# Optimization experiments

Measured on AMD Instinct MI355X. Metric: run time of the kernel, lower is better.

The kernel has to match this reference:

```python
import jax, jax.numpy as jnp
import numpy as np

D_MODEL = 2048
D_STATE = 16
EXPAND = 2
D_INNER = D_MODEL * EXPAND
BATCH = 2048
LN_EPS = 1e-5


def setup_inputs() -> dict:
    key = jax.random.key(0)
    ks = jax.random.split(key, 8)
    x = jax.random.normal(ks[0], (BATCH, D_MODEL), dtype=jnp.float32)
    h = jax.random.normal(ks[1], (BATCH, D_INNER, D_STATE), dtype=jnp.float32)
    # Learned parameters (Linear weights stored as (out, in), torch convention)
    W_in = jax.random.normal(ks[2], (2 * D_INNER, D_MODEL), dtype=jnp.float32) / np.sqrt(D_MODEL)
    W_xp = jax.random.normal(ks[3], (2 * D_STATE + 1, D_INNER), dtype=jnp.float32) / np.sqrt(D_INNER)
    log_A = -jnp.log(jnp.arange(1, D_STATE + 1, dtype=jnp.float32))[None, :] * jnp.ones((D_INNER, 1), jnp.float32)
    dt_bias = jax.random.normal(ks[4], (D_INNER,), dtype=jnp.float32) * 0.01 - 2.0
    D_param = jnp.ones((D_INNER,), dtype=jnp.float32)
    W_out = jax.random.normal(ks[5], (D_MODEL, D_INNER), dtype=jnp.float32) / np.sqrt(D_INNER)
    gamma = jnp.ones((D_MODEL,), dtype=jnp.float32)
    beta = jnp.zeros((D_MODEL,), dtype=jnp.float32)
    return {"x": x, "h": h, "W_in": W_in, "W_xp": W_xp, "log_A": log_A,
            "dt_bias": dt_bias, "D_param": D_param, "W_out": W_out,
            "gamma": gamma, "beta": beta}


def reference(x, h, W_in, W_xp, log_A, dt_bias, D_param, W_out, gamma, beta):
    d_state = log_A.shape[1]
    residual = x
    # LayerNorm
    mu = jnp.mean(x, axis=-1, keepdims=True)
    var = jnp.mean(jnp.square(x - mu), axis=-1, keepdims=True)
    xn = (x - mu) / jnp.sqrt(var + LN_EPS) * gamma + beta
    # in_proj -> split into main stream and gate
    xz = xn @ W_in.T                       # (B, 2*d_inner)
    x_main, z = jnp.split(xz, 2, axis=-1)  # each (B, d_inner)
    # selective projections: B_t, C_t, delta
    xp = x_main @ W_xp.T                   # (B, 2*d_state+1)
    B_t = xp[:, :d_state]                  # (B, d_state)
    C_t = xp[:, d_state:2 * d_state]       # (B, d_state)
    delta_raw = xp[:, -1]                  # (B,)
    delta = jax.nn.softplus(delta_raw[:, None] + dt_bias)  # (B, d_inner)
    A = jnp.exp(log_A)                     # (d_inner, d_state)
    A_bar = jnp.exp(-delta[:, :, None] * A)              # (B, d_inner, d_state)
    B_bar = delta[:, :, None] * B_t[:, None, :]          # (B, d_inner, d_state)
    h_new = A_bar * h + B_bar * x_main[:, :, None]       # (B, d_inner, d_state)
    y_ssm = jnp.sum(h_new * C_t[:, None, :], axis=-1) + D_param * x_main  # (B, d_inner)
    y_gated = y_ssm * jax.nn.silu(z)
    y = y_gated @ W_out.T + residual       # (B, d_model)
    return (y, h_new)
```

## Files before the change

kernel.cpp:

```cpp
#include <hip/hip_runtime.h>
#include <cstddef>

#define BATCH 2048
#define DM 2048
#define DI 4096
#define DS 16
#define LN_EPS 1e-5f

typedef __bf16 bf16x8 __attribute__((ext_vector_type(8)));
typedef float f32x4 __attribute__((ext_vector_type(4)));
typedef unsigned short u16;

__device__ __forceinline__ u16 f2bf(float f) {
  unsigned u = __float_as_uint(f);
  u += 0x7fffu + ((u >> 16) & 1u);
  return (u16)(u >> 16);
}
__device__ __forceinline__ void split1(float f, u16& h, u16& l) {
  h = f2bf(f);
  float hf = __uint_as_float((unsigned)h << 16);
  l = f2bf(f - hf);
}

#define GLOAD16(g, l)                                                          \
  __builtin_amdgcn_global_load_lds(                                            \
      (const __attribute__((address_space(1))) unsigned int*)(g),              \
      (__attribute__((address_space(3))) unsigned int*)(l), 16, 0, 0)

__global__ __launch_bounds__(256) void ln_split_kernel(
    const float* __restrict__ x, const float* __restrict__ gamma,
    const float* __restrict__ beta, u16* __restrict__ xnh,
    u16* __restrict__ xnl) {
  int row = blockIdx.x;
  int t = threadIdx.x;
  const float4* xr = (const float4*)(x + (size_t)row * DM);
  float4 v0 = xr[t];
  float4 v1 = xr[t + 256];
  float s  = v0.x + v0.y + v0.z + v0.w + v1.x + v1.y + v1.z + v1.w;
  float ss = v0.x*v0.x + v0.y*v0.y + v0.z*v0.z + v0.w*v0.w
           + v1.x*v1.x + v1.y*v1.y + v1.z*v1.z + v1.w*v1.w;
#pragma unroll
  for (int off = 32; off >= 1; off >>= 1) {
    s  += __shfl_down(s, off);
    ss += __shfl_down(ss, off);
  }
  __shared__ float red[8];
  int wave = t >> 6;
  if ((t & 63) == 0) { red[wave] = s; red[4 + wave] = ss; }
  __syncthreads();
  if (t == 0) {
    float fs  = red[0] + red[1] + red[2] + red[3];
    float fss = red[4] + red[5] + red[6] + red[7];
    float mu  = fs * (1.0f / DM);
    red[0] = mu;
    red[1] = rsqrtf(fss * (1.0f / DM) - mu * mu + LN_EPS);
  }
  __syncthreads();
  float mu = red[0], rstd = red[1];
  const float4* g  = (const float4*)gamma;
  const float4* be = (const float4*)beta;
  float4 g0 = g[t], g1 = g[t + 256], b0 = be[t], b1 = be[t + 256];
  float o[8];
  o[0] = (v0.x - mu) * rstd * g0.x + b0.x;
  o[1] = (v0.y - mu) * rstd * g0.y + b0.y;
  o[2] = (v0.z - mu) * rstd * g0.z + b0.z;
  o[3] = (v0.w - mu) * rstd * g0.w + b0.w;
  o[4] = (v1.x - mu) * rstd * g1.x + b1.x;
  o[5] = (v1.y - mu) * rstd * g1.y + b1.y;
  o[6] = (v1.z - mu) * rstd * g1.z + b1.z;
  o[7] = (v1.w - mu) * rstd * g1.w + b1.w;
  ushort4 h0, l0, h1, l1;
  split1(o[0], h0.x, l0.x); split1(o[1], h0.y, l0.y);
  split1(o[2], h0.z, l0.z); split1(o[3], h0.w, l0.w);
  split1(o[4], h1.x, l1.x); split1(o[5], h1.y, l1.y);
  split1(o[6], h1.z, l1.z); split1(o[7], h1.w, l1.w);
  ushort4* hr = (ushort4*)(xnh + (size_t)row * DM);
  ushort4* lr = (ushort4*)(xnl + (size_t)row * DM);
  hr[t] = h0; hr[t + 256] = h1;
  lr[t] = l0; lr[t + 256] = l1;
}

__global__ __launch_bounds__(256) void split_kernel(const float* __restrict__ in,
                                                    u16* __restrict__ hi,
                                                    u16* __restrict__ lo,
                                                    int n4) {
  int i = blockIdx.x * 256 + threadIdx.x;
  if (i >= n4) return;
  float4 v = ((const float4*)in)[i];
  ushort4 h, l;
  split1(v.x, h.x, l.x); split1(v.y, h.y, l.y);
  split1(v.z, h.z, l.z); split1(v.w, h.w, l.w);
  ((ushort4*)hi)[i] = h;
  ((ushort4*)lo)[i] = l;
}

template <int BN>
__global__ __launch_bounds__(256) void gemm_split(
    const u16* __restrict__ Ah, const u16* __restrict__ Al,
    const u16* __restrict__ Bh, const u16* __restrict__ Bl,
    float* __restrict__ C, const float* __restrict__ resid,
    int M, int N, int K) {
  (void)M;
  constexpr int NF = BN / 32;
  constexpr int BPART = BN * 64;
  __shared__ alignas(16) char lds[16384 + 2 * BPART];

  const int t = threadIdx.x;
  const int lane = t & 63;
  const int w = t >> 6;
  const int bm = blockIdx.y << 7;
  const int bn = blockIdx.x * BN;
  const int wr = (w >> 1) << 6;
  const int wc = (w & 1) * (NF * 16);

  const int sr = t >> 2;
  const int kc_s = (t & 3) ^ (sr & 3);
  const size_t oA0 = (size_t)(bm + sr) * K + kc_s * 8;
  const size_t oA1 = oA0 + (size_t)64 * K;
  const size_t oB0 = (size_t)(bn + sr) * K + kc_s * 8;
  const size_t oB1 = oB0 + (size_t)64 * K;
  char* l0 = lds + (w << 10);

  const int lrow = lane & 15;
  const int kq = lane >> 4;
  const int ksw = ((kq ^ (lrow & 3)) << 4);
  int foA[4], foB[NF];
#pragma unroll
  for (int i = 0; i < 4; ++i) foA[i] = (wr + i * 16 + lrow) * 64 + ksw;
#pragma unroll
  for (int j = 0; j < NF; ++j) foB[j] = (wc + j * 16 + lrow) * 64 + ksw;

  f32x4 acc[4][NF];
#pragma unroll
  for (int i = 0; i < 4; ++i)
#pragma unroll
    for (int j = 0; j < NF; ++j) acc[i][j] = (f32x4){0.f, 0.f, 0.f, 0.f};

  for (int k0 = 0; k0 < K; k0 += 32) {
    __syncthreads();
    GLOAD16(Ah + oA0 + k0, l0);
    GLOAD16(Ah + oA1 + k0, l0 + 4096);
    GLOAD16(Al + oA0 + k0, l0 + 8192);
    GLOAD16(Al + oA1 + k0, l0 + 8192 + 4096);
    GLOAD16(Bh + oB0 + k0, l0 + 16384);
    GLOAD16(Bl + oB0 + k0, l0 + 16384 + BPART);
    if constexpr (BN == 128) {
      GLOAD16(Bh + oB1 + k0, l0 + 16384 + 4096);
      GLOAD16(Bl + oB1 + k0, l0 + 16384 + BPART + 4096);
    }
    __syncthreads();

    bf16x8 ah[4], al4[4], bh[NF], bl4[NF];
#pragma unroll
    for (int i = 0; i < 4; ++i) {
      ah[i]  = *(const bf16x8*)(lds + foA[i]);
      al4[i] = *(const bf16x8*)(lds + 8192 + foA[i]);
    }
#pragma unroll
    for (int j = 0; j < NF; ++j) {
      bh[j]  = *(const bf16x8*)(lds + 16384 + foB[j]);
      bl4[j] = *(const bf16x8*)(lds + 16384 + BPART + foB[j]);
    }
#pragma unroll
    for (int i = 0; i < 4; ++i)
#pragma unroll
      for (int j = 0; j < NF; ++j) {
        acc[i][j] = __builtin_amdgcn_mfma_f32_16x16x32_bf16(ah[i],  bh[j],  acc[i][j], 0, 0, 0);
        acc[i][j] = __builtin_amdgcn_mfma_f32_16x16x32_bf16(ah[i],  bl4[j], acc[i][j], 0, 0, 0);
        acc[i][j] = __builtin_amdgcn_mfma_f32_16x16x32_bf16(al4[i], bh[j],  acc[i][j], 0, 0, 0);
      }
  }

  const int rb = bm + wr + (kq << 2);
  const int cb = bn + wc + lrow;
#pragma unroll
  for (int i = 0; i < 4; ++i) {
#pragma unroll
    for (int r = 0; r < 4; ++r) {
      const size_t ro = (size_t)(rb + i * 16 + r) * N + cb;
#pragma unroll
      for (int j = 0; j < NF; ++j) {
        float v = acc[i][j][r];
        if (resid) v += resid[ro + j * 16];
        C[ro + j * 16] = v;
      }
    }
  }
}

__global__ __launch_bounds__(256) void xp_kernel(const float* __restrict__ xz,
                                                 const float* __restrict__ W_xp,
                                                 float* __restrict__ xp) {
  int b = blockIdx.x;
  int t = threadIdx.x;
  const float* xm = xz + ((size_t)b << 13);
  float acc[33];
#pragma unroll
  for (int j = 0; j < 33; ++j) acc[j] = 0.f;
  for (int k = t; k < DI; k += 256) {
    float xv = xm[k];
#pragma unroll
    for (int j = 0; j < 33; ++j)
      acc[j] = fmaf(xv, W_xp[j * DI + k], acc[j]);
  }
#pragma unroll
  for (int j = 0; j < 33; ++j) {
#pragma unroll
    for (int off = 32; off >= 1; off >>= 1)
      acc[j] += __shfl_down(acc[j], off);
  }
  __shared__ float red[4][33];
  int wave = t >> 6, lane = t & 63;
  if (lane == 0) {
#pragma unroll
    for (int j = 0; j < 33; ++j) red[wave][j] = acc[j];
  }
  __syncthreads();
  if (t < 33)
    xp[b * 33 + t] = red[0][t] + red[1][t] + red[2][t] + red[3][t];
}

__global__ __launch_bounds__(256) void ssm_kernel(const float* __restrict__ xz,
                                                  const float* __restrict__ xp,
                                                  const float* __restrict__ h,
                                                  const float* __restrict__ log_A,
                                                  const float* __restrict__ dt_bias,
                                                  const float* __restrict__ D_param,
                                                  float* __restrict__ h_new,
                                                  u16* __restrict__ ygh,
                                                  u16* __restrict__ ygl) {
  size_t idx = (size_t)blockIdx.x * 256 + threadIdx.x;
  int b = (int)(idx >> 12);
  int d = (int)(idx & 4095);
  const float* xrow = xz + ((size_t)b << 13);
  float xm = xrow[d];
  float zv = xrow[4096 + d];
  const float* xpb = xp + b * 33;
  float tt = xpb[32] + dt_bias[d];
  float delta = (tt > 0.f) ? tt + log1pf(__expf(-tt)) : log1pf(__expf(tt));
  float dxm = delta * xm;
  const float4* hp  = (const float4*)(h + (idx << 4));
  const float4* lap = (const float4*)(log_A + ((size_t)d << 4));
  float4* hop = (float4*)(h_new + (idx << 4));
  float y = 0.f;
#pragma unroll
  for (int q = 0; q < 4; ++q) {
    float4 hv = hp[q];
    float4 la = lap[q];
    float B0 = xpb[q * 4 + 0], B1 = xpb[q * 4 + 1];
    float B2 = xpb[q * 4 + 2], B3 = xpb[q * 4 + 3];
    float C0 = xpb[16 + q * 4 + 0], C1 = xpb[16 + q * 4 + 1];
    float C2 = xpb[16 + q * 4 + 2], C3 = xpb[16 + q * 4 + 3];
    float4 hn;
    hn.x = __expf(-delta * __expf(la.x)) * hv.x + B0 * dxm;
    hn.y = __expf(-delta * __expf(la.y)) * hv.y + B1 * dxm;
    hn.z = __expf(-delta * __expf(la.z)) * hv.z + B2 * dxm;
    hn.w = __expf(-delta * __expf(la.w)) * hv.w + B3 * dxm;
    y = fmaf(hn.x, C0, y);
    y = fmaf(hn.y, C1, y);
    y = fmaf(hn.z, C2, y);
    y = fmaf(hn.w, C3, y);
    hop[q] = hn;
  }
  y = fmaf(D_param[d], xm, y);
  float sig = 1.0f / (1.0f + __expf(-zv));
  float yv = y * (zv * sig);
  u16 hs, ls;
  split1(yv, hs, ls);
  ygh[idx] = hs;
  ygl[idx] = ls;
}

extern "C" void kernel_launch(void* const* d_in, const int* in_sizes, int n_in,
                              void* d_out, int out_size, void* d_ws, size_t ws_size,
                              hipStream_t stream) {
  const float* x       = (const float*)d_in[0];
  const float* h       = (const float*)d_in[1];
  const float* W_in    = (const float*)d_in[2];
  const float* W_xp    = (const float*)d_in[3];
  const float* log_A   = (const float*)d_in[4];
  const float* dt_bias = (const float*)d_in[5];
  const float* D_param = (const float*)d_in[6];
  const float* W_out   = (const float*)d_in[7];
  const float* gamma   = (const float*)d_in[8];
  const float* beta    = (const float*)d_in[9];

  float* out   = (float*)d_out;
  float* y_out = out;
  float* h_out = out + (size_t)BATCH * DM;

  float* ws  = (float*)d_ws;
  float* xz  = ws;
  float* xpb = xz + (size_t)BATCH * 2 * DI;
  u16*  ygh  = (u16*)(xpb + (size_t)BATCH * 33);
  u16*  ygl  = ygh + (size_t)BATCH * DI;

  u16* xnh = (u16*)y_out;
  u16* xnl = xnh + (size_t)BATCH * DM;
  u16* Wih = (u16*)h_out;
  u16* Wil = Wih + (size_t)2 * DI * DM;
  u16* Woh = (u16*)xz;
  u16* Wol = Woh + (size_t)DM * DI;

  ln_split_kernel<<<BATCH, 256, 0, stream>>>(x, gamma, beta, xnh, xnl);
  split_kernel<<<(2 * DI * DM / 4) / 256, 256, 0, stream>>>(
      W_in, Wih, Wil, 2 * DI * DM / 4);
  gemm_split<128><<<dim3((2 * DI) / 128, BATCH / 128), 256, 0, stream>>>(
      xnh, xnl, Wih, Wil, xz, nullptr, BATCH, 2 * DI, DM);
  xp_kernel<<<BATCH, 256, 0, stream>>>(xz, W_xp, xpb);
  ssm_kernel<<<(BATCH * DI) / 256, 256, 0, stream>>>(
      xz, xpb, h, log_A, dt_bias, D_param, h_out, ygh, ygl);
  split_kernel<<<(DM * DI / 4) / 256, 256, 0, stream>>>(
      W_out, Woh, Wol, DM * DI / 4);
  gemm_split<64><<<dim3(DM / 64, BATCH / 128), 256, 0, stream>>>(
      ygh, ygl, Woh, Wol, y_out, x, BATCH, DM, DI);
}
```

Measured before the change: 1.530 ms.

## Swizzle GEMM block order and spread SSM state over four lanes

The GEMM remaps its linear block id with an XCD-style swizzle, so consecutive workgroups on the same die share A/B tiles in L2. The SSM kernel now gives each (batch, channel) pair four threads, one float4 of state each, and combines their partial outputs with shuffles. Adjacent lanes then touch adjacent float4s of h, which should coalesce the dominant h read and h_new write and raise parallelism. The cost is four times as many threads, each repeating the softplus and scalar loads.

```diff
diff --git a/kernel.cpp b/kernel.cpp
--- a/kernel.cpp
+++ b/kernel.cpp
@@ -108,8 +108,14 @@
   const int t = threadIdx.x;
   const int lane = t & 63;
   const int w = t >> 6;
-  const int bm = blockIdx.y << 7;
-  const int bn = blockIdx.x * BN;
+
+  const int nbx = gridDim.x;
+  const int nwg = nbx * gridDim.y;
+  const int bid = blockIdx.y * nbx + blockIdx.x;
+  const int swz = (bid & 7) * (nwg >> 3) + (bid >> 3);
+  const int bm = (swz / nbx) << 7;
+  const int bn = (swz % nbx) * BN;
+
   const int wr = (w >> 1) << 6;
   const int wc = (w & 1) * (NF * 16);
 
@@ -229,46 +235,45 @@
                                                   float* __restrict__ h_new,
                                                   u16* __restrict__ ygh,
                                                   u16* __restrict__ ygl) {
-  size_t idx = (size_t)blockIdx.x * 256 + threadIdx.x;
-  int b = (int)(idx >> 12);
-  int d = (int)(idx & 4095);
+  size_t tid = (size_t)blockIdx.x * 256 + threadIdx.x;
+  size_t g = tid >> 2;
+  int q = (int)(tid & 3);
+  int b = (int)(g >> 12);
+  int d = (int)(g & 4095);
   const float* xrow = xz + ((size_t)b << 13);
   float xm = xrow[d];
-  float zv = xrow[4096 + d];
   const float* xpb = xp + b * 33;
   float tt = xpb[32] + dt_bias[d];
   float delta = (tt > 0.f) ? tt + log1pf(__expf(-tt)) : log1pf(__expf(tt));
   float dxm = delta * xm;
-  const float4* hp  = (const float4*)(h + (idx << 4));
-  const float4* lap = (const float4*)(log_A + ((size_t)d << 4));
-  float4* hop = (float4*)(h_new + (idx << 4));
-  float y = 0.f;
-#pragma unroll
-  for (int q = 0; q < 4; ++q) {
-    float4 hv = hp[q];
-    float4 la = lap[q];
-    float B0 = xpb[q * 4 + 0], B1 = xpb[q * 4 + 1];
-    float B2 = xpb[q * 4 + 2], B3 = xpb[q * 4 + 3];
-    float C0 = xpb[16 + q * 4 + 0], C1 = xpb[16 + q * 4 + 1];
-    float C2 = xpb[16 + q * 4 + 2], C3 = xpb[16 + q * 4 + 3];
-    float4 hn;
-    hn.x = __expf(-delta * __expf(la.x)) * hv.x + B0 * dxm;
-    hn.y = __expf(-delta * __expf(la.y)) * hv.y + B1 * dxm;
-    hn.z = __expf(-delta * __expf(la.z)) * hv.z + B2 * dxm;
-    hn.w = __expf(-delta * __expf(la.w)) * hv.w + B3 * dxm;
-    y = fmaf(hn.x, C0, y);
-    y = fmaf(hn.y, C1, y);
-    y = fmaf(hn.z, C2, y);
-    y = fmaf(hn.w, C3, y);
-    hop[q] = hn;
-  }
-  y = fmaf(D_param[d], xm, y);
-  float sig = 1.0f / (1.0f + __expf(-zv));
-  float yv = y * (zv * sig);
-  u16 hs, ls;
-  split1(yv, hs, ls);
-  ygh[idx] = hs;
-  ygl[idx] = ls;
+  float4 hv = ((const float4*)h)[g * 4 + q];
+  float4 la = ((const float4*)log_A)[((size_t)d << 2) + q];
+  float B0 = xpb[q * 4 + 0], B1 = xpb[q * 4 + 1];
+  float B2 = xpb[q * 4 + 2], B3 = xpb[q * 4 + 3];
+  float C0 = xpb[16 + q * 4 + 0], C1 = xpb[16 + q * 4 + 1];
+  float C2 = xpb[16 + q * 4 + 2], C3 = xpb[16 + q * 4 + 3];
+  float4 hn;
+  hn.x = __expf(-delta * __expf(la.x)) * hv.x + B0 * dxm;
+  hn.y = __expf(-delta * __expf(la.y)) * hv.y + B1 * dxm;
+  hn.z = __expf(-delta * __expf(la.z)) * hv.z + B2 * dxm;
+  hn.w = __expf(-delta * __expf(la.w)) * hv.w + B3 * dxm;
+  ((float4*)h_new)[g * 4 + q] = hn;
+  float y = hn.x * C0;
+  y = fmaf(hn.y, C1, y);
+  y = fmaf(hn.z, C2, y);
+  y = fmaf(hn.w, C3, y);
+  y += __shfl_xor(y, 1);
+  y += __shfl_xor(y, 2);
+  if (q == 0) {
+    float zv = xrow[4096 + d];
+    y = fmaf(D_param[d], xm, y);
+    float sig = 1.0f / (1.0f + __expf(-zv));
+    float yv = y * (zv * sig);
+    u16 hs, ls;
+    split1(yv, hs, ls);
+    ygh[g] = hs;
+    ygl[g] = ls;
+  }
 }
 
 extern "C" void kernel_launch(void* const* d_in, const int* in_sizes, int n_in,
@@ -308,7 +313,7 @@
   gemm_split<128><<<dim3((2 * DI) / 128, BATCH / 128), 256, 0, stream>>>(
       xnh, xnl, Wih, Wil, xz, nullptr, BATCH, 2 * DI, DM);
   xp_kernel<<<BATCH, 256, 0, stream>>>(xz, W_xp, xpb);
-  ssm_kernel<<<(BATCH * DI) / 256, 256, 0, stream>>>(
+  ssm_kernel<<<(BATCH * DI * 4) / 256, 256, 0, stream>>>(
       xz, xpb, h, log_A, dt_bias, D_param, h_out, ygh, ygl);
   split_kernel<<<(DM * DI / 4) / 256, 256, 0, stream>>>(
       W_out, Woh, Wol, DM * DI / 4);
```

After: 1.429 ms. 1.07x faster.
